# Optimization experiments

Measured on AMD Instinct MI355X. Metric: run time of the kernel, lower is better.

## Reference

```python
import jax, jax.numpy as jnp
import numpy as np

B, S, D = 4, 2048, 1024
H, DH = 16, 64  # d_model = H*DH = 1024
NEG = 1e10


def setup_inputs() -> dict:
    key = jax.random.key(0)
    ks = jax.random.split(key, 5)
    scale = 1.0 / np.sqrt(D)
    x = jax.random.normal(ks[0], (B, S, D), dtype=jnp.float32)
    mask = jax.random.randint(ks[1], (B, S), 0, 2).astype(jnp.float32)
    Wq = jax.random.normal(ks[2], (D, H * DH), dtype=jnp.float32) * scale
    Wk = jax.random.normal(ks[3], (D, H * DH), dtype=jnp.float32) * scale
    Wv = jax.random.normal(ks[4], (D, H * DH), dtype=jnp.float32) * scale
    z = jnp.zeros((H * DH,), dtype=jnp.float32)
    return {"x": x, "mask": mask, "Wq": Wq, "bq": z, "Wk": Wk, "bk": z,
            "Wv": Wv, "bv": z}


def reference(x, mask, Wq, bq, Wk, bk, Wv, bv):
    # projections -> [B, H, S, DH]
    def proj(W, b):
        y = x @ W + b
        return y.reshape(B, S, H, DH).transpose(0, 2, 1, 3)

    q, k, v = proj(Wq, bq), proj(Wk, bk), proj(Wv, bv)
    scores = jnp.einsum("bhsd,bhtd->bhst", q, k) / np.sqrt(DH)
    m = mask[:, None, None, :]                      # [B,1,1,S]
    scores = scores - (1.0 - m) * NEG               # additive mask
    probs = jax.nn.softmax(scores, axis=-1)         # stable (max-subtract)
    probs = probs * m                               # multiplicative mask
    out = jnp.einsum("bhst,bhtd->bhsd", probs, v)   # [B,H,S,DH]
    return out.transpose(0, 2, 1, 3).reshape(B, S, H * DH)
```

## Files before the change

### kernel.cpp

```cpp
#include <hip/hip_runtime.h>

typedef float f32x4 __attribute__((ext_vector_type(4)));
typedef float f32x16 __attribute__((ext_vector_type(16)));
typedef _Float16 f16;
typedef _Float16 f16x2 __attribute__((ext_vector_type(2)));
typedef _Float16 f16x8 __attribute__((ext_vector_type(8)));
typedef unsigned int u32x2 __attribute__((ext_vector_type(2)));
typedef unsigned short u16;
typedef unsigned int u32;

#define S_LEN 2048
#define NHEAD 16
#define DHEAD 64
#define DMODEL 1024
#define NBATCH 4

__device__ __forceinline__ void gload16(const u16* g, const uint4* l) {
  __builtin_amdgcn_global_load_lds((const __attribute__((address_space(1))) void*)g,
                                   (__attribute__((address_space(3))) void*)l, 16, 0, 0);
}


__global__ void cvt_x(const float* __restrict__ x, u16* __restrict__ o, int n4) {
  int i = blockIdx.x * blockDim.x + threadIdx.x;
  int st = gridDim.x * blockDim.x;
  for (; i < n4; i += st) {
    float4 v = reinterpret_cast<const float4*>(x)[i];
    uint2 r;
    r.x = __builtin_bit_cast(u32, __builtin_amdgcn_cvt_pkrtz(v.x, v.y));
    r.y = __builtin_bit_cast(u32, __builtin_amdgcn_cvt_pkrtz(v.z, v.w));
    reinterpret_cast<uint2*>(o)[i] = r;
  }
}

__global__ void trans_w(const float* __restrict__ W, u16* __restrict__ wt) {
  __shared__ float t[32][33];
  int bx = blockIdx.x * 32, by = blockIdx.y * 32;
  int tx = threadIdx.x & 31, ty = threadIdx.x >> 5;
#pragma unroll
  for (int i = 0; i < 32; i += 8)
    t[ty + i][tx] = W[(size_t)(by + ty + i) * DMODEL + bx + tx];
  __syncthreads();
#pragma unroll
  for (int i = 0; i < 32; i += 8)
    wt[(size_t)(bx + ty + i) * DMODEL + by + tx] = __builtin_bit_cast(u16, (f16)t[tx][ty + i]);
}

__global__ __launch_bounds__(256) void qkv_gemm(
    const u16* __restrict__ A, const u16* __restrict__ Wt,
    const float* __restrict__ bq, const float* __restrict__ bk, const float* __restrict__ bv,
    const float* __restrict__ mask,
    u16* __restrict__ Qo, u16* __restrict__ Ko, u16* __restrict__ Vo)
{
  __shared__ uint4 As4[3][512];
  __shared__ uint4 Bs4[3][512];
  const int tid = threadIdx.x;
  const int lane = tid & 63;
  const int wid = tid >> 6;
  const int l15 = lane & 15, l4 = lane >> 4;
  const int m0 = blockIdx.x * 128;
  const int n0 = blockIdx.y * 128;
  const int wr = (wid >> 1) * 64, wc = (wid & 1) * 64;

  f32x4 acc[4][4];
#pragma unroll
  for (int m = 0; m < 4; m++)
#pragma unroll
    for (int n = 0; n < 4; n++) { acc[m][n][0]=0.f; acc[m][n][1]=0.f; acc[m][n][2]=0.f; acc[m][n][3]=0.f; }

  const int c0 = wid * 64 + lane, c1 = c0 + 256;
  const int r0 = c0 >> 2, r1 = c1 >> 2;
  const int p4 = lane & 3;
  const int sl0 = p4 ^ ((r0 >> 1) & 3);
  const int sl1 = p4 ^ ((r1 >> 1) & 3);
  const u16* ag0 = A  + (size_t)(m0 + r0) * 1024 + sl0 * 8;
  const u16* ag1 = A  + (size_t)(m0 + r1) * 1024 + sl1 * 8;
  const u16* bg0 = Wt + (size_t)(n0 + r0) * 1024 + sl0 * 8;
  const u16* bg1 = Wt + (size_t)(n0 + r1) * 1024 + sl1 * 8;

  auto stage = [&](int buf, int kt) {
    gload16(ag0 + kt, &As4[buf][wid * 64]);
    gload16(ag1 + kt, &As4[buf][wid * 64 + 256]);
    gload16(bg0 + kt, &Bs4[buf][wid * 64]);
    gload16(bg1 + kt, &Bs4[buf][wid * 64 + 256]);
  };

  stage(0, 0);
  stage(1, 32);
  __syncthreads();

  const int NT = 1024 / 32;
  for (int it = 0; it < NT; ++it) {
    if (it + 1 < NT) asm volatile("s_waitcnt vmcnt(4)" ::: "memory");
    else             asm volatile("s_waitcnt vmcnt(0)" ::: "memory");
    __builtin_amdgcn_s_barrier();
    __builtin_amdgcn_sched_barrier(0);
    const int cur = it % 3;
    if (it + 2 < NT) stage((it + 2) % 3, (it + 2) * 32);

    const u16* As = (const u16*)&As4[cur][0];
    const u16* Bs = (const u16*)&Bs4[cur][0];
    f16x8 a[4], b[4];
#pragma unroll
    for (int m = 0; m < 4; m++) {
      int r = wr + m * 16 + l15;
      a[m] = *(const f16x8*)&As[r * 32 + (l4 ^ ((r >> 1) & 3)) * 8];
    }
#pragma unroll
    for (int n = 0; n < 4; n++) {
      int r = wc + n * 16 + l15;
      b[n] = *(const f16x8*)&Bs[r * 32 + (l4 ^ ((r >> 1) & 3)) * 8];
    }
#pragma unroll
    for (int m = 0; m < 4; m++)
#pragma unroll
      for (int n = 0; n < 4; n++)
        acc[m][n] = __builtin_amdgcn_mfma_f32_16x16x32_f16(a[m], b[n], acc[m][n], 0, 0, 0);
  }

  const int sel = n0 >> 10;
  const float* bias = (sel == 0) ? bq : (sel == 1) ? bk : bv;
  const int nbase = (n0 & 1023) + wc;
  const float QSCALE = 0.18033688011112042f;
#pragma unroll
  for (int m = 0; m < 4; m++)
#pragma unroll
    for (int n = 0; n < 4; n++)
#pragma unroll
      for (int j = 0; j < 4; j++) {
        int row  = m0 + wr + m * 16 + l4 * 4 + j;
        int ncol = nbase + n * 16 + l15;
        float v = acc[m][n][j] + bias[ncol];
        int bb = row >> 11, s = row & 2047;
        int h = ncol >> 6, dh = ncol & 63;
        size_t bh = (size_t)(bb * NHEAD + h);
        if (sel == 0)      Qo[(bh * S_LEN + s) * DHEAD + dh] = __builtin_bit_cast(u16, (f16)(v * QSCALE));
        else if (sel == 1) Ko[(bh * S_LEN + s) * DHEAD + dh] = __builtin_bit_cast(u16, (f16)v);
        else {
          if (mask[bb * S_LEN + s] <= 0.f) v = 0.f;
          Vo[(bh * DHEAD + dh) * S_LEN + s] = __builtin_bit_cast(u16, (f16)v);
        }
      }
}

__global__ __launch_bounds__(256, 2) void attn(
    const u16* __restrict__ Q, const u16* __restrict__ K, const u16* __restrict__ Vt,
    const float* __restrict__ mask, float* __restrict__ out)
{
  __shared__ uint4 Ks4[3][512];
  __shared__ uint4 Vs4[3][512];
  __shared__ __align__(16) u16 MsAll[S_LEN];
  const int tid = threadIdx.x;
  const int lane = tid & 63, wid = tid >> 6;
  const int l31 = lane & 31, hi = lane >> 5;
  const int sid = blockIdx.x;
  const int qt = (sid >> 3) & 7;
  const int bh = (sid & 7) + 8 * (sid >> 6);
  const int b = bh >> 4, h = bh & 15;
  const size_t base = (size_t)bh * S_LEN * DHEAD;
  const u16* Qp = Q + base;
  const u16* Kp = K + base;
  const u16* Vp = Vt + base;
  const float* mp = mask + b * S_LEN;
  const int q0 = qt * 256 + wid * 64;

  f16x8 aqA[4], aqB[4];
#pragma unroll
  for (int kc = 0; kc < 4; kc++) {
    aqA[kc] = *(const f16x8*)&Qp[(size_t)(q0 + l31) * DHEAD + kc * 16 + hi * 8];
    aqB[kc] = *(const f16x8*)&Qp[(size_t)(q0 + 32 + l31) * DHEAD + kc * 16 + hi * 8];
  }

  f32x16 accO0A = {}, accO1A = {}, accLA = {};
  f32x16 accO0B = {}, accO1B = {}, accLB = {};

  const int cA_ = wid * 128 + lane, cB_ = cA_ + 64;
  const int rk0 = cA_ >> 3, rk1 = cB_ >> 3;
  const int p8 = lane & 7;
  const int cc0 = (p8 - ((rk0 + (rk0 >> 3)) & 7)) & 7;
  const int cc1 = (p8 - ((rk1 + (rk1 >> 3)) & 7)) & 7;
  const u16* kg0 = Kp + (size_t)rk0 * DHEAD + cc0 * 8;
  const u16* kg1 = Kp + (size_t)rk1 * DHEAD + cc1 * 8;
  const u16* vg0 = Vp + (size_t)rk0 * S_LEN + cc0 * 8;
  const u16* vg1 = Vp + (size_t)rk1 * S_LEN + cc1 * 8;

  auto stage = [&](int buf) {
    gload16(kg0, &Ks4[buf][wid * 128]); gload16(kg1, &Ks4[buf][wid * 128 + 64]);
    gload16(vg0, &Vs4[buf][wid * 128]); gload16(vg1, &Vs4[buf][wid * 128 + 64]);
    kg0 += 64 * DHEAD; kg1 += 64 * DHEAD; vg0 += 64; vg1 += 64;
  };

  const int swA = (l31 + (l31 >> 3)) & 7;
  const int swB = (swA + 4) & 7;
  int idxA[4], idxB[4];
#pragma unroll
  for (int kc = 0; kc < 4; kc++) {
    idxA[kc] = l31 * 8 + ((kc * 2 + hi + swA) & 7);
    idxB[kc] = (32 + l31) * 8 + ((kc * 2 + hi + swB) & 7);
  }

  {
    float4 ml0 = *(const float4*)&mp[tid * 8];
    float4 ml1 = *(const float4*)&mp[tid * 8 + 4];
    uint4 w;
    w.x = __builtin_bit_cast(u32, __builtin_amdgcn_cvt_pkrtz(ml0.x, ml0.y));
    w.y = __builtin_bit_cast(u32, __builtin_amdgcn_cvt_pkrtz(ml0.z, ml0.w));
    w.z = __builtin_bit_cast(u32, __builtin_amdgcn_cvt_pkrtz(ml1.x, ml1.y));
    w.w = __builtin_bit_cast(u32, __builtin_amdgcn_cvt_pkrtz(ml1.z, ml1.w));
    *(uint4*)&MsAll[tid * 8] = w;
  }
  stage(0);
  stage(1);
  __syncthreads();

  const int NT = S_LEN / 64;
  for (int it = 0; it < NT; ++it) {
    if (it + 1 < NT) asm volatile("s_waitcnt vmcnt(4)" ::: "memory");
    else             asm volatile("s_waitcnt vmcnt(0)" ::: "memory");
    __builtin_amdgcn_s_barrier();
    __builtin_amdgcn_sched_barrier(0);
    const int cur = it % 3;
    const uint4* ks = &Ks4[cur][0];
    const uint4* vs = &Vs4[cur][0];
    if (it + 2 < NT) stage((it + 2) % 3);

    f32x16 sA0 = {}, sA1 = {}, sB0 = {}, sB1 = {};
#pragma unroll
    for (int kc = 0; kc < 4; kc++) {
      f16x8 k0 = *(const f16x8*)&ks[idxA[kc]];
      f16x8 k1 = *(const f16x8*)&ks[idxB[kc]];
      sA0 = __builtin_amdgcn_mfma_f32_32x32x16_f16(k0, aqA[kc], sA0, 0, 0, 0);
      sA1 = __builtin_amdgcn_mfma_f32_32x32x16_f16(k1, aqA[kc], sA1, 0, 0, 0);
      sB0 = __builtin_amdgcn_mfma_f32_32x32x16_f16(k0, aqB[kc], sB0, 0, 0, 0);
      sB1 = __builtin_amdgcn_mfma_f32_32x32x16_f16(k1, aqB[kc], sB1, 0, 0, 0);
    }

#pragma unroll
    for (int g = 0; g < 4; g++) {
      const f32x16& srcA = (g < 2) ? sA0 : sA1;
      const f32x16& srcB = (g < 2) ? sB0 : sB1;
      const int o = (g & 1) * 8;
      u32 wa[4], wb[4];
#pragma unroll
      for (int s = 0; s < 4; s++) {
        wa[s] = __builtin_bit_cast(u32, __builtin_amdgcn_cvt_pkrtz(
                    __builtin_amdgcn_exp2f(srcA[o + 2 * s]),
                    __builtin_amdgcn_exp2f(srcA[o + 2 * s + 1])));
        wb[s] = __builtin_bit_cast(u32, __builtin_amdgcn_cvt_pkrtz(
                    __builtin_amdgcn_exp2f(srcB[o + 2 * s]),
                    __builtin_amdgcn_exp2f(srcB[o + 2 * s + 1])));
      }
      u32x2 rA0 = __builtin_amdgcn_permlane32_swap(wa[0], wa[2], false, false);
      u32x2 rA1 = __builtin_amdgcn_permlane32_swap(wa[1], wa[3], false, false);
      u32x2 rB0 = __builtin_amdgcn_permlane32_swap(wb[0], wb[2], false, false);
      u32x2 rB1 = __builtin_amdgcn_permlane32_swap(wb[1], wb[3], false, false);
      uint4 f4A; f4A.x = rA0[0]; f4A.y = rA1[0]; f4A.z = rA0[1]; f4A.w = rA1[1];
      uint4 f4B; f4B.x = rB0[0]; f4B.y = rB1[0]; f4B.z = rB0[1]; f4B.w = rB1[1];
      f16x8 fA = __builtin_bit_cast(f16x8, f4A);
      f16x8 fB = __builtin_bit_cast(f16x8, f4B);
      f16x8 bv0 = *(const f16x8*)&vs[idxA[g]];
      f16x8 bv1 = *(const f16x8*)&vs[idxB[g]];
      f16x8 bm = *(const f16x8*)&MsAll[it * 64 + g * 16 + hi * 8];
      accO0A = __builtin_amdgcn_mfma_f32_32x32x16_f16(fA, bv0, accO0A, 0, 0, 0);
      accO1A = __builtin_amdgcn_mfma_f32_32x32x16_f16(fA, bv1, accO1A, 0, 0, 0);
      accLA  = __builtin_amdgcn_mfma_f32_32x32x16_f16(fA, bm,  accLA,  0, 0, 0);
      accO0B = __builtin_amdgcn_mfma_f32_32x32x16_f16(fB, bv0, accO0B, 0, 0, 0);
      accO1B = __builtin_amdgcn_mfma_f32_32x32x16_f16(fB, bv1, accO1B, 0, 0, 0);
      accLB  = __builtin_amdgcn_mfma_f32_32x32x16_f16(fB, bm,  accLB,  0, 0, 0);
    }
  }

#pragma unroll
  for (int r = 0; r < 16; r++) {
    int qr = (r & 3) + 8 * (r >> 2) + 4 * hi;
    float lA = accLA[r], lB = accLB[r];
    float iA = (lA > 0.f) ? 1.f / lA : 0.f;
    float iB = (lB > 0.f) ? 1.f / lB : 0.f;
    float* opA = out + ((size_t)(b * S_LEN + q0 + qr) * DMODEL) + h * DHEAD;
    float* opB = out + ((size_t)(b * S_LEN + q0 + 32 + qr) * DMODEL) + h * DHEAD;
    opA[l31] = accO0A[r] * iA;
    opA[32 + l31] = accO1A[r] * iA;
    opB[l31] = accO0B[r] * iB;
    opB[32 + l31] = accO1B[r] * iB;
  }
}

extern "C" void kernel_launch(void* const* d_in, const int* in_sizes, int n_in,
                              void* d_out, int out_size, void* d_ws, size_t ws_size,
                              hipStream_t stream) {
  const float* x    = (const float*)d_in[0];
  const float* mask = (const float*)d_in[1];
  const float* Wq   = (const float*)d_in[2];
  const float* bq   = (const float*)d_in[3];
  const float* Wk   = (const float*)d_in[4];
  const float* bk   = (const float*)d_in[5];
  const float* Wv   = (const float*)d_in[6];
  const float* bv   = (const float*)d_in[7];
  float* out = (float*)d_out;

  u16* xb = (u16*)d_ws;
  u16* wt = xb + (size_t)8192 * 1024;
  u16* Qb = wt + (size_t)3072 * 1024;
  u16* Kb = Qb + (size_t)8388608;
  u16* Vb = Kb + (size_t)8388608;

  cvt_x<<<2048, 256, 0, stream>>>(x, xb, (8192 * 1024) / 4);
  trans_w<<<dim3(32, 32), 256, 0, stream>>>(Wq, wt);
  trans_w<<<dim3(32, 32), 256, 0, stream>>>(Wk, wt + (size_t)1024 * 1024);
  trans_w<<<dim3(32, 32), 256, 0, stream>>>(Wv, wt + (size_t)2 * 1024 * 1024);
  qkv_gemm<<<dim3(64, 24), 256, 0, stream>>>(xb, wt, bq, bk, bv, mask, Qb, Kb, Vb);
  attn<<<512, 256, 0, stream>>>(Qb, Kb, Vb, mask, out);
}
```

Before: 174.2 us.

## Retile QKV GEMM to 256x256 blocks with 32x32 MFMA and deeper pipeline

The QKV projection GEMM moves from 128x128 tiles on 256 threads to 256x256 tiles on 512 threads. It switches to 32x32x16 MFMA instructions, uses a 4-stage LDS ring with three tiles prefetched instead of two, and applies a 1D grid with a swizzled block order. LDS offsets are precomputed, and the V-transpose epilogue writes packed 4-element stores. The aim is more data reuse per LDS load and better latency hiding, at the cost of 128KB of LDS per block and fewer blocks (384) across the CUs.

```diff
diff --git a/kernel.cpp b/kernel.cpp
--- a/kernel.cpp
+++ b/kernel.cpp
@@ -7,6 +7,7 @@
 typedef _Float16 f16x8 __attribute__((ext_vector_type(8)));
 typedef unsigned int u32x2 __attribute__((ext_vector_type(2)));
 typedef unsigned short u16;
+typedef unsigned short u16x4 __attribute__((ext_vector_type(4)));
 typedef unsigned int u32;
 
 #define S_LEN 2048
@@ -46,31 +47,32 @@
     wt[(size_t)(bx + ty + i) * DMODEL + by + tx] = __builtin_bit_cast(u16, (f16)t[tx][ty + i]);
 }
 
-__global__ __launch_bounds__(256) void qkv_gemm(
+__global__ __launch_bounds__(512, 2) void qkv_gemm(
     const u16* __restrict__ A, const u16* __restrict__ Wt,
     const float* __restrict__ bq, const float* __restrict__ bk, const float* __restrict__ bv,
     const float* __restrict__ mask,
     u16* __restrict__ Qo, u16* __restrict__ Ko, u16* __restrict__ Vo)
 {
-  __shared__ uint4 As4[3][512];
-  __shared__ uint4 Bs4[3][512];
+  __shared__ uint4 As4[4][1024];
+  __shared__ uint4 Bs4[4][1024];
   const int tid = threadIdx.x;
   const int lane = tid & 63;
   const int wid = tid >> 6;
-  const int l15 = lane & 15, l4 = lane >> 4;
-  const int m0 = blockIdx.x * 128;
-  const int n0 = blockIdx.y * 128;
-  const int wr = (wid >> 1) * 64, wc = (wid & 1) * 64;
-
-  f32x4 acc[4][4];
-#pragma unroll
-  for (int m = 0; m < 4; m++)
-#pragma unroll
-    for (int n = 0; n < 4; n++) { acc[m][n][0]=0.f; acc[m][n][1]=0.f; acc[m][n][2]=0.f; acc[m][n][3]=0.f; }
-
-  const int c0 = wid * 64 + lane, c1 = c0 + 256;
-  const int r0 = c0 >> 2, r1 = c1 >> 2;
-  const int p4 = lane & 3;
+  const int l31 = lane & 31, hi = lane >> 5;
+
+  const int id = blockIdx.x;
+  const int swz = (id & 7) * 48 + (id >> 3);
+  const int m0 = (swz & 31) * 256;
+  const int n0 = (swz >> 5) * 256;
+
+  const int wrM = (wid >> 2) * 128;
+  const int wcN = (wid & 3) * 64;
+
+  f32x16 acc[4][2] = {};
+
+  const int r0 = tid >> 2;
+  const int r1 = r0 + 128;
+  const int p4 = tid & 3;
   const int sl0 = p4 ^ ((r0 >> 1) & 3);
   const int sl1 = p4 ^ ((r1 >> 1) & 3);
   const u16* ag0 = A  + (size_t)(m0 + r0) * 1024 + sl0 * 8;
@@ -79,68 +81,104 @@
   const u16* bg1 = Wt + (size_t)(n0 + r1) * 1024 + sl1 * 8;
 
   auto stage = [&](int buf, int kt) {
-    gload16(ag0 + kt, &As4[buf][wid * 64]);
-    gload16(ag1 + kt, &As4[buf][wid * 64 + 256]);
-    gload16(bg0 + kt, &Bs4[buf][wid * 64]);
-    gload16(bg1 + kt, &Bs4[buf][wid * 64 + 256]);
+    gload16(ag0 + kt * 32, &As4[buf][wid * 64]);
+    gload16(ag1 + kt * 32, &As4[buf][wid * 64 + 512]);
+    gload16(bg0 + kt * 32, &Bs4[buf][wid * 64]);
+    gload16(bg1 + kt * 32, &Bs4[buf][wid * 64 + 512]);
   };
 
+  int aoff[4][2], boff[2][2];
+#pragma unroll
+  for (int mi = 0; mi < 4; mi++) {
+    int r = wrM + mi * 32 + l31;
+#pragma unroll
+    for (int ks = 0; ks < 2; ks++)
+      aoff[mi][ks] = r * 32 + (((ks * 2 + hi) ^ ((r >> 1) & 3)) * 8);
+  }
+#pragma unroll
+  for (int ni = 0; ni < 2; ni++) {
+    int r = wcN + ni * 32 + l31;
+#pragma unroll
+    for (int ks = 0; ks < 2; ks++)
+      boff[ni][ks] = r * 32 + (((ks * 2 + hi) ^ ((r >> 1) & 3)) * 8);
+  }
+
   stage(0, 0);
-  stage(1, 32);
+  stage(1, 1);
+  stage(2, 2);
   __syncthreads();
 
   const int NT = 1024 / 32;
   for (int it = 0; it < NT; ++it) {
-    if (it + 1 < NT) asm volatile("s_waitcnt vmcnt(4)" ::: "memory");
-    else             asm volatile("s_waitcnt vmcnt(0)" ::: "memory");
+    if (it + 2 < NT)      asm volatile("s_waitcnt vmcnt(8)" ::: "memory");
+    else if (it + 1 < NT) asm volatile("s_waitcnt vmcnt(4)" ::: "memory");
+    else                  asm volatile("s_waitcnt vmcnt(0)" ::: "memory");
     __builtin_amdgcn_s_barrier();
     __builtin_amdgcn_sched_barrier(0);
-    const int cur = it % 3;
-    if (it + 2 < NT) stage((it + 2) % 3, (it + 2) * 32);
+    const int cur = it & 3;
+    if (it + 3 < NT) stage((it + 3) & 3, it + 3);
 
     const u16* As = (const u16*)&As4[cur][0];
     const u16* Bs = (const u16*)&Bs4[cur][0];
-    f16x8 a[4], b[4];
-#pragma unroll
-    for (int m = 0; m < 4; m++) {
-      int r = wr + m * 16 + l15;
-      a[m] = *(const f16x8*)&As[r * 32 + (l4 ^ ((r >> 1) & 3)) * 8];
-    }
-#pragma unroll
-    for (int n = 0; n < 4; n++) {
-      int r = wc + n * 16 + l15;
-      b[n] = *(const f16x8*)&Bs[r * 32 + (l4 ^ ((r >> 1) & 3)) * 8];
-    }
-#pragma unroll
-    for (int m = 0; m < 4; m++)
-#pragma unroll
-      for (int n = 0; n < 4; n++)
-        acc[m][n] = __builtin_amdgcn_mfma_f32_16x16x32_f16(a[m], b[n], acc[m][n], 0, 0, 0);
+    f16x8 af[4][2], bf[2][2];
+#pragma unroll
+    for (int mi = 0; mi < 4; mi++)
+#pragma unroll
+      for (int ks = 0; ks < 2; ks++)
+        af[mi][ks] = *(const f16x8*)&As[aoff[mi][ks]];
+#pragma unroll
+    for (int ni = 0; ni < 2; ni++)
+#pragma unroll
+      for (int ks = 0; ks < 2; ks++)
+        bf[ni][ks] = *(const f16x8*)&Bs[boff[ni][ks]];
+
+#pragma unroll
+    for (int ks = 0; ks < 2; ks++)
+#pragma unroll
+      for (int mi = 0; mi < 4; mi++)
+#pragma unroll
+        for (int ni = 0; ni < 2; ni++)
+          acc[mi][ni] = __builtin_amdgcn_mfma_f32_32x32x16_f16(af[mi][ks], bf[ni][ks], acc[mi][ni], 0, 0, 0);
   }
 
   const int sel = n0 >> 10;
   const float* bias = (sel == 0) ? bq : (sel == 1) ? bk : bv;
-  const int nbase = (n0 & 1023) + wc;
+  const int nb = (n0 & 1023) + wcN;
   const float QSCALE = 0.18033688011112042f;
 #pragma unroll
-  for (int m = 0; m < 4; m++)
-#pragma unroll
-    for (int n = 0; n < 4; n++)
-#pragma unroll
-      for (int j = 0; j < 4; j++) {
-        int row  = m0 + wr + m * 16 + l4 * 4 + j;
-        int ncol = nbase + n * 16 + l15;
-        float v = acc[m][n][j] + bias[ncol];
-        int bb = row >> 11, s = row & 2047;
-        int h = ncol >> 6, dh = ncol & 63;
-        size_t bh = (size_t)(bb * NHEAD + h);
-        if (sel == 0)      Qo[(bh * S_LEN + s) * DHEAD + dh] = __builtin_bit_cast(u16, (f16)(v * QSCALE));
-        else if (sel == 1) Ko[(bh * S_LEN + s) * DHEAD + dh] = __builtin_bit_cast(u16, (f16)v);
-        else {
-          if (mask[bb * S_LEN + s] <= 0.f) v = 0.f;
-          Vo[(bh * DHEAD + dh) * S_LEN + s] = __builtin_bit_cast(u16, (f16)v);
+  for (int mi = 0; mi < 4; mi++)
+#pragma unroll
+    for (int ni = 0; ni < 2; ni++) {
+      const int ncol = nb + ni * 32 + l31;
+      const float bi = bias[ncol];
+      const int h = ncol >> 6, dh = ncol & 63;
+#pragma unroll
+      for (int r4 = 0; r4 < 4; r4++) {
+        const int rowb = m0 + wrM + mi * 32 + 8 * r4 + 4 * hi;
+        const int bb = rowb >> 11, s0 = rowb & 2047;
+        const size_t bh = (size_t)(bb * NHEAD + h);
+        if (sel == 0) {
+#pragma unroll
+          for (int j = 0; j < 4; j++)
+            Qo[(bh * S_LEN + s0 + j) * DHEAD + dh] =
+                __builtin_bit_cast(u16, (f16)((acc[mi][ni][r4 * 4 + j] + bi) * QSCALE));
+        } else if (sel == 1) {
+#pragma unroll
+          for (int j = 0; j < 4; j++)
+            Ko[(bh * S_LEN + s0 + j) * DHEAD + dh] =
+                __builtin_bit_cast(u16, (f16)(acc[mi][ni][r4 * 4 + j] + bi));
+        } else {
+          u16x4 pk;
+#pragma unroll
+          for (int j = 0; j < 4; j++) {
+            float v = acc[mi][ni][r4 * 4 + j] + bi;
+            if (mask[bb * S_LEN + s0 + j] <= 0.f) v = 0.f;
+            pk[j] = __builtin_bit_cast(u16, (f16)v);
+          }
+          *(u16x4*)&Vo[(bh * DHEAD + dh) * S_LEN + s0] = pk;
         }
       }
+    }
 }
 
 __global__ __launch_bounds__(256, 2) void attn(
@@ -308,6 +346,6 @@
   trans_w<<<dim3(32, 32), 256, 0, stream>>>(Wq, wt);
   trans_w<<<dim3(32, 32), 256, 0, stream>>>(Wk, wt + (size_t)1024 * 1024);
   trans_w<<<dim3(32, 32), 256, 0, stream>>>(Wv, wt + (size_t)2 * 1024 * 1024);
-  qkv_gemm<<<dim3(64, 24), 256, 0, stream>>>(xb, wt, bq, bk, bv, mask, Qb, Kb, Vb);
+  qkv_gemm<<<dim3(384), 512, 0, stream>>>(xb, wt, bq, bk, bv, mask, Qb, Kb, Vb);
   attn<<<512, 256, 0, stream>>>(Qb, Kb, Vb, mask, out);
 }
```

Result: slower. 190.2 us (+9.2%).
